# Optimization experiments

Hardware: AMD Instinct MI355X
Metric: run time of the kernel (lower is better)

Reference implementation:

```python
import jax, jax.numpy as jnp
import numpy as np
import math

N = 4096      # nodes
E = 131072    # edges
D = 256       # hidden / out_features
DIN = 16      # distance_map feature dim
H = 2         # attention heads
HD = D // H   # head dim = 128


def setup_inputs() -> dict:
    key = jax.random.key(0)
    ks = jax.random.split(key, 20)
    s = 0.02
    return {
        "input": jax.random.normal(ks[0], (N, D), jnp.float32),
        "adj": jax.random.randint(ks[1], (2, E), 0, N, jnp.int64),
        "h0": jax.random.normal(ks[2], (N, D), jnp.float32),
        "lamda": 1,
        "alpha": jax.random.uniform(ks[3], (1,), jnp.float32),
        "l": 1,
        "distance_map": jax.random.normal(ks[4], (E, DIN), jnp.float32),
        "norm": jax.random.uniform(ks[5], (E,), jnp.float32),
        # GraphConvolution params
        "weight_local": jax.random.normal(ks[6], (2 * D, D), jnp.float32) * s,
        "weight_global": jax.random.normal(ks[7], (2 * D, D), jnp.float32) * s,
        # EA_GCN.lin : Linear(16, D)
        "lin_w": jax.random.normal(ks[8], (D, DIN), jnp.float32) * s,
        "lin_b": jnp.zeros((D,), jnp.float32),
        # EA_GCN.W_EV : 3D -> 2D -> D -> 16 (GELU between)
        "w1": jax.random.normal(ks[9], (2 * D, 3 * D), jnp.float32) * s,
        "b1": jnp.zeros((2 * D,), jnp.float32),
        "w2": jax.random.normal(ks[10], (D, 2 * D), jnp.float32) * s,
        "b2": jnp.zeros((D,), jnp.float32),
        "w3": jax.random.normal(ks[11], (DIN, D), jnp.float32) * s,
        "b3": jnp.zeros((DIN,), jnp.float32),
        # MultiheadAttention params (torch layout: in_proj [3D, D])
        "in_proj_w": jax.random.normal(ks[12], (3 * D, D), jnp.float32) * s,
        "in_proj_b": jnp.zeros((3 * D,), jnp.float32),
        "out_proj_w": jax.random.normal(ks[13], (D, D), jnp.float32) * s,
        "out_proj_b": jnp.zeros((D,), jnp.float32),
    }


def _mha(x, wi, bi, wo, bo):
    # torch MHA, unbatched (N, D) input, eval mode (dropout off)
    qkv = x @ wi.T + bi                      # [N, 3D]
    q, k, v = jnp.split(qkv, 3, axis=-1)
    q = q.reshape(N, H, HD).transpose(1, 0, 2)  # [H, N, HD]
    k = k.reshape(N, H, HD).transpose(1, 0, 2)
    v = v.reshape(N, H, HD).transpose(1, 0, 2)
    scores = jnp.einsum("hnd,hmd->hnm", q, k) / math.sqrt(HD)
    attn = jax.nn.softmax(scores, axis=-1)
    o = jnp.einsum("hnm,hmd->hnd", attn, v)     # [H, N, HD]
    o = o.transpose(1, 0, 2).reshape(N, D)
    return o @ wo.T + bo


def _ea_gcn(x, edge_index, norm, distance_map, lin_w, lin_b, w1, b1, w2, b2, w3, b3):
    src, dst = edge_index[0], edge_index[1]
    edge_attr = distance_map @ lin_w.T + lin_b               # [E, D]
    msg = norm[:, None] * (x[src] + edge_attr)               # gather + combine
    agg = jax.ops.segment_sum(msg, dst, num_segments=N)      # scatter-add
    x_out = agg + x
    h = jnp.concatenate([x_out[src], edge_attr, x_out[dst]], axis=-1)  # [E, 3D]
    h = jax.nn.gelu(h @ w1.T + b1, approximate=False)
    h = jax.nn.gelu(h @ w2.T + b2, approximate=False)
    dm_out = h @ w3.T + b3                                   # [E, 16]
    return x_out, dm_out


def reference(input, adj, h0, lamda, alpha, l, distance_map, norm,
              weight_local, weight_global, lin_w, lin_b,
              w1, b1, w2, b2, w3, b3,
              in_proj_w, in_proj_b, out_proj_w, out_proj_b):
    theta = min(1.0, math.log(lamda / l + 1.0))
    a = alpha[0]
    h_local, dm_out = _ea_gcn(input, adj, norm, distance_map,
                              lin_w, lin_b, w1, b1, w2, b2, w3, b3)
    h_global = _mha(input, in_proj_w, in_proj_b, out_proj_w, out_proj_b)
    support_local = jnp.concatenate([h_local, h0], axis=1)   # [N, 2D]
    r_local = (1.0 - a) * h_local + a * h0
    support_global = jnp.concatenate([h_global, h0], axis=1)
    r_global = (1.0 - a) * h_global + a * h0
    output_local = theta * (support_local @ weight_local) + (1.0 - theta) * r_local
    output_global = theta * (support_global @ weight_global) + (1.0 - theta) * r_global
    output = output_local + output_global                    # residual=False
    return (output, dm_out)
```

## Files before the change

kernel.cpp:

```cpp
#include <hip/hip_runtime.h>
#include <hip/hip_bf16.h>
#include <math.h>

constexpr int N_   = 4096;
constexpr int E_   = 131072;
constexpr int D_   = 256;
constexpr int DIN_ = 16;
constexpr int D3_  = 768;
constexpr int HD_  = 128;

typedef __bf16 bf16_8 __attribute__((ext_vector_type(8)));
typedef float  f32x4  __attribute__((ext_vector_type(4)));
typedef float  f32x4v __attribute__((ext_vector_type(4)));
typedef unsigned int u32x4 __attribute__((ext_vector_type(4)));

__device__ __forceinline__ unsigned short f2b(float f) {
  unsigned int u = __float_as_uint(f);
  u = u + 0x7fffu + ((u >> 16) & 1u);
  return (unsigned short)(u >> 16);
}
__device__ __forceinline__ float b2f(unsigned short s) {
  return __uint_as_float(((unsigned int)s) << 16);
}
__device__ __forceinline__ unsigned int pack2(unsigned short lo, unsigned short hi) {
// ... 256 lines not shown
    const unsigned short* __restrict__ inb, const unsigned short* __restrict__ wqb,
    const float* __restrict__ ipb, float* __restrict__ qkv) {
  __shared__ unsigned short sA[128][72];
  __shared__ unsigned short sB[128][72];
  const int b   = blockIdx.x;
  const int j0  = (b % 6) * 128;
  const int m0  = (b / 6) * 128;
  const int tid = threadIdx.x;
  const int lane = tid & 63, wv = tid >> 6;
  const int r16  = lane & 15, quad = lane >> 4;
  const int sr   = tid >> 1, sh = (tid & 1) * 32;

  const unsigned short* ra = inb + (size_t)(m0 + sr) * D_;
  const unsigned short* rb = wqb + (size_t)(j0 + sr) * D_;

  const f32x4 zz = {0.f, 0.f, 0.f, 0.f};
  f32x4 acc[2][8];
#pragma unroll
  for (int m = 0; m < 2; ++m)
#pragma unroll
    for (int n = 0; n < 8; ++n) acc[m][n] = zz;

  for (int ki = 0; ki < 4; ++ki) {
    __syncthreads();
    {
      const uint4* s    = (const uint4*)(ra + ki * 64 + sh);
      const uint4* bsrc = (const uint4*)(rb + ki * 64 + sh);
      uint4* da = (uint4*)&sA[sr][sh];
      uint4* db = (uint4*)&sB[sr][sh];
#pragma unroll
      for (int i = 0; i < 4; ++i) { da[i] = s[i]; db[i] = bsrc[i]; }
    }
    __syncthreads();
#pragma unroll
    for (int kk = 0; kk < 2; ++kk) {
      bf16_8 a0 = frag16(&sA[wv * 32 + r16][kk * 32 + quad * 8]);
      bf16_8 a1 = frag16(&sA[wv * 32 + 16 + r16][kk * 32 + quad * 8]);
#pragma unroll
      for (int n = 0; n < 8; ++n) {
        bf16_8 bf = frag16(&sB[n * 16 + r16][kk * 32 + quad * 8]);
        acc[0][n] = __builtin_amdgcn_mfma_f32_16x16x32_bf16(a0, bf, acc[0][n], 0, 0, 0);
        acc[1][n] = __builtin_amdgcn_mfma_f32_16x16x32_bf16(a1, bf, acc[1][n], 0, 0, 0);
      }
    }
  }
#pragma unroll
  for (int m = 0; m < 2; ++m)
#pragma unroll
    for (int n = 0; n < 8; ++n) {
      int col = j0 + n * 16 + r16;
      float bb = ipb[col];
#pragma unroll
      for (int rg = 0; rg < 4; ++rg) {
        int row = m0 + wv * 32 + m * 16 + quad * 4 + rg;
        qkv[(size_t)row * D3_ + col] = acc[m][n][rg] + bb;
      }
    }
}

__global__ __launch_bounds__(256) void k_node_pac(
    const unsigned short* __restrict__ xbp, const unsigned short* __restrict__ wb1,
    unsigned short* __restrict__ Pac) {
  __shared__ unsigned short sA[128][72];
  __shared__ unsigned short sB[128][72];
  const int b    = blockIdx.x;
  const int j0   = (b & 7) * 128;
  const int m0   = (b >> 3) * 128;
  const int side = j0 >> 9;
  const int jr   = j0 - side * 512;
  const int tid  = threadIdx.x;
  const int lane = tid & 63, wv = tid >> 6;
  const int r16  = lane & 15, quad = lane >> 4;
  const int sr   = tid >> 1, sh = (tid & 1) * 32;

  const unsigned short* ra = xbp + (size_t)(m0 + sr) * D_;
  const unsigned short* rb = wb1 + (size_t)(jr + sr) * 768 + side * 512;

  const f32x4 zz = {0.f, 0.f, 0.f, 0.f};
  f32x4 acc[2][8];
#pragma unroll
  for (int m = 0; m < 2; ++m)
#pragma unroll
    for (int n = 0; n < 8; ++n) acc[m][n] = zz;

  for (int ki = 0; ki < 4; ++ki) {
    __syncthreads();
    {
      const uint4* s    = (const uint4*)(ra + ki * 64 + sh);
      const uint4* bsrc = (const uint4*)(rb + ki * 64 + sh);
      uint4* da = (uint4*)&sA[sr][sh];
      uint4* db = (uint4*)&sB[sr][sh];
#pragma unroll
      for (int i = 0; i < 4; ++i) { da[i] = s[i]; db[i] = bsrc[i]; }
    }
    __syncthreads();
#pragma unroll
    for (int kk = 0; kk < 2; ++kk) {
      bf16_8 a0 = frag16(&sA[wv * 32 + r16][kk * 32 + quad * 8]);
      bf16_8 a1 = frag16(&sA[wv * 32 + 16 + r16][kk * 32 + quad * 8]);
#pragma unroll
      for (int n = 0; n < 8; ++n) {
        bf16_8 bf = frag16(&sB[n * 16 + r16][kk * 32 + quad * 8]);
        acc[0][n] = __builtin_amdgcn_mfma_f32_16x16x32_bf16(a0, bf, acc[0][n], 0, 0, 0);
        acc[1][n] = __builtin_amdgcn_mfma_f32_16x16x32_bf16(a1, bf, acc[1][n], 0, 0, 0);
      }
    }
  }
#pragma unroll
  for (int m = 0; m < 2; ++m)
#pragma unroll
    for (int n = 0; n < 8; ++n) {
      int col = j0 + n * 16 + r16;
#pragma unroll
      for (int rg = 0; rg < 4; ++rg) {
        int row = m0 + wv * 32 + m * 16 + quad * 4 + rg;
        Pac[(size_t)row * 1024 + col] = f2b(acc[m][n][rg]);
      }
    }
}

__global__ __launch_bounds__(256) void k_outproj_mfma(
    const unsigned short* __restrict__ attob, const unsigned short* __restrict__ opwb,
    const float* __restrict__ opb, float* __restrict__ hgl,
    unsigned short* __restrict__ hgb) {
  __shared__ unsigned short sA[128][72];
  __shared__ unsigned short sB[128][72];
  const int b   = blockIdx.x;
  const int j0  = (b & 1) * 128;
  const int m0  = (b >> 1) * 128;
  const int tid = threadIdx.x;
  const int lane = tid & 63, wv = tid >> 6;
  const int r16  = lane & 15, quad = lane >> 4;
  const int sr   = tid >> 1, sh = (tid & 1) * 32;

  const unsigned short* ra = attob + (size_t)(m0 + sr) * D_;
  const unsigned short* rb = opwb + (size_t)(j0 + sr) * D_;

  const f32x4 zz = {0.f, 0.f, 0.f, 0.f};
  f32x4 acc[2][8];
#pragma unroll
  for (int m = 0; m < 2; ++m)
#pragma unroll
    for (int n = 0; n < 8; ++n) acc[m][n] = zz;

  for (int ki = 0; ki < 4; ++ki) {
    __syncthreads();
    {
      const uint4* s    = (const uint4*)(ra + ki * 64 + sh);
      const uint4* bsrc = (const uint4*)(rb + ki * 64 + sh);
      uint4* da = (uint4*)&sA[sr][sh];
      uint4* db = (uint4*)&sB[sr][sh];
#pragma unroll
      for (int i = 0; i < 4; ++i) { da[i] = s[i]; db[i] = bsrc[i]; }
    }
    __syncthreads();
#pragma unroll
    for (int kk = 0; kk < 2; ++kk) {
      bf16_8 a0 = frag16(&sA[wv * 32 + r16][kk * 32 + quad * 8]);
      bf16_8 a1 = frag16(&sA[wv * 32 + 16 + r16][kk * 32 + quad * 8]);
#pragma unroll
      for (int n = 0; n < 8; ++n) {
        bf16_8 bf = frag16(&sB[n * 16 + r16][kk * 32 + quad * 8]);
        acc[0][n] = __builtin_amdgcn_mfma_f32_16x16x32_bf16(a0, bf, acc[0][n], 0, 0, 0);
        acc[1][n] = __builtin_amdgcn_mfma_f32_16x16x32_bf16(a1, bf, acc[1][n], 0, 0, 0);
      }
    }
  }
#pragma unroll
  for (int m = 0; m < 2; ++m)
#pragma unroll
    for (int n = 0; n < 8; ++n) {
      int col = j0 + n * 16 + r16;
      float bb = opb[col];
#pragma unroll
      for (int rg = 0; rg < 4; ++rg) {
        int row = m0 + wv * 32 + m * 16 + quad * 4 + rg;
        float v = acc[m][n][rg] + bb;
        size_t idx = (size_t)row * D_ + col;
        hgl[idx] = v;
        hgb[idx] = f2b(v);
      }
    }
}

__global__ __launch_bounds__(256) void k_final_mfma(
    const unsigned short* __restrict__ xbp, const unsigned short* __restrict__ h0b,
    const unsigned short* __restrict__ hgb,
    const unsigned short* __restrict__ wlT, const unsigned short* __restrict__ wgT,
    const float* __restrict__ hl, const float* __restrict__ hg, const float* __restrict__ h0,
    const float* __restrict__ alpha_p, const void* lamda_p, const void* l_p,
    float* __restrict__ out) {
  __shared__ unsigned short sA[128][72];
  __shared__ unsigned short sB[128][72];
  const int b   = blockIdx.x;
  const int j0  = (b & 1) * 128;
  const int m0  = (b >> 1) * 128;
  const int tid = threadIdx.x;
  const int lane = tid & 63, wv = tid >> 6;
  const int r16  = lane & 15, quad = lane >> 4;
  const int sr   = tid >> 1, sh = (tid & 1) * 32;

  const f32x4 zz = {0.f, 0.f, 0.f, 0.f};
  f32x4 acc[2][8];
#pragma unroll
  for (int m = 0; m < 2; ++m)
#pragma unroll
    for (int n = 0; n < 8; ++n) acc[m][n] = zz;

  const size_t arow = (size_t)(m0 + sr) * D_;
  const size_t brow = (size_t)(j0 + sr) * 512;

  for (int ki = 0; ki < 16; ++ki) {
    __syncthreads();
    {
      const int gc = ki * 64 + sh;
      const unsigned short* ap =
          (gc < 256) ? xbp + arow + gc
        : (gc < 512) ? h0b + arow + (gc - 256)
        : (gc < 768) ? hgb + arow + (gc - 512)
                     : h0b + arow + (gc - 768);
      const unsigned short* bp = (gc < 512) ? wlT + brow + gc : wgT + brow + (gc - 512);
      const uint4* s    = (const uint4*)ap;
      const uint4* bsrc = (const uint4*)bp;
      uint4* da = (uint4*)&sA[sr][sh];
      uint4* db = (uint4*)&sB[sr][sh];
#pragma unroll
      for (int i = 0; i < 4; ++i) { da[i] = s[i]; db[i] = bsrc[i]; }
    }
    __syncthreads();
#pragma unroll
    for (int kk = 0; kk < 2; ++kk) {
      bf16_8 a0 = frag16(&sA[wv * 32 + r16][kk * 32 + quad * 8]);
      bf16_8 a1 = frag16(&sA[wv * 32 + 16 + r16][kk * 32 + quad * 8]);
#pragma unroll
      for (int n = 0; n < 8; ++n) {
        bf16_8 bf = frag16(&sB[n * 16 + r16][kk * 32 + quad * 8]);
        acc[0][n] = __builtin_amdgcn_mfma_f32_16x16x32_bf16(a0, bf, acc[0][n], 0, 0, 0);
        acc[1][n] = __builtin_amdgcn_mfma_f32_16x16x32_bf16(a1, bf, acc[1][n], 0, 0, 0);
      }
    }
  }
  float theta = fminf(1.f, logf(scalar_as_float(lamda_p) / scalar_as_float(l_p) + 1.f));
  float a = alpha_p[0];
  float omt = 1.f - theta;
#pragma unroll
  for (int m = 0; m < 2; ++m)
#pragma unroll
    for (int n = 0; n < 8; ++n) {
      int col = j0 + n * 16 + r16;
#pragma unroll
      for (int rg = 0; rg < 4; ++rg) {
        int row = m0 + wv * 32 + m * 16 + quad * 4 + rg;
        size_t idx = (size_t)row * D_ + col;
        out[idx] = theta * acc[m][n][rg] +
                   omt * ((1.f - a) * (hl[idx] + hg[idx]) + 2.f * a * h0[idx]);
      }
    }
}

__global__ void k_qk2b(const float* __restrict__ qkv,
                       unsigned short* __restrict__ Qb, unsigned short* __restrict__ Kb) {
  int off = (blockIdx.x * 256 + threadIdx.x) * 8;
  int n = off >> 9, c = off & 511;
  const float* src = qkv + (size_t)n * D3_ + c;
  float4 a = *(const float4*)src;
  float4 b = *(const float4*)(src + 4);
  uint4 p = {pack2(f2b(a.x), f2b(a.y)), pack2(f2b(a.z), f2b(a.w)),
             pack2(f2b(b.x), f2b(b.y)), pack2(f2b(b.z), f2b(b.w))};
  int cc = c & 255;
  int hh = cc >> 7, d = cc & 127;
  unsigned short* dst = (c < 256 ? Qb : Kb) + (size_t)hh * N_ * HD_ + (size_t)n * HD_ + d;
  *(uint4*)dst = p;
}

__global__ __launch_bounds__(256) void k_v2t(const float* __restrict__ qkv,
                                             unsigned short* __restrict__ Vt) {
  __shared__ unsigned short sv[64][136];
  int h = blockIdx.y;
  int n0 = blockIdx.x * 64;
  int tid = threadIdx.x;
#pragma unroll
  for (int it = 0; it < 4; ++it) {
    int off = (tid + it * 256) * 8;
    int r = off >> 7, d = off & 127;
    const float* src = qkv + (size_t)(n0 + r) * D3_ + 2 * D_ + h * HD_ + d;
    float4 a = *(const float4*)src;
    float4 b = *(const float4*)(src + 4);
    uint4 p = {pack2(f2b(a.x), f2b(a.y)), pack2(f2b(a.z), f2b(a.w)),
               pack2(f2b(b.x), f2b(b.y)), pack2(f2b(b.z), f2b(b.w))};
    *(uint4*)&sv[r][d] = p;
  }
  __syncthreads();
#pragma unroll
  for (int it = 0; it < 4; ++it) {
    int off = (tid + it * 256) * 8;
    int d = off >> 6, k = off & 63;
    unsigned short t[8];
#pragma unroll
    for (int j = 0; j < 8; ++j) t[j] = sv[k + j][d];
    uint4 p = {pack2(t[0], t[1]), pack2(t[2], t[3]),
               pack2(t[4], t[5]), pack2(t[6], t[7])};
    *(uint4*)(Vt + (size_t)h * HD_ * N_ + (size_t)d * N_ + n0 + k) = p;
  }
}

__global__ __launch_bounds__(256) void k_attn_mfma(
    const unsigned short* __restrict__ Qb, const unsigned short* __restrict__ Kb,
    const unsigned short* __restrict__ Vt, float* __restrict__ o_out,
    unsigned short* __restrict__ ob) {
  __shared__ unsigned short sK[64][136];
  __shared__ unsigned short sV[128][72];
  __shared__ float          sS[16][68];
  __shared__ unsigned short sP[16][72];
  __shared__ float sm[16], sl[16], sa[16];

  const int tid  = threadIdx.x;
  const int h    = blockIdx.y;
  const int q0   = blockIdx.x * 16;
  const int lane = tid & 63;
  const int wv   = tid >> 6;
  const int r16  = lane & 15;
  const int quad = lane >> 4;

  bf16_8 qf[4];
#pragma unroll
  for (int kk = 0; kk < 4; ++kk)
    qf[kk] = frag16(Qb + (size_t)h * N_ * HD_ + (size_t)(q0 + r16) * HD_ + kk * 32 + quad * 8);

  if (tid < 16) { sm[tid] = -1e30f; sl[tid] = 0.f; }

  const f32x4 zz = {0.f, 0.f, 0.f, 0.f};
  f32x4 o0 = zz, o1 = zz;

  const unsigned short* Kh = Kb + (size_t)h * N_ * HD_;
  const unsigned short* Vh = Vt + (size_t)h * HD_ * N_;

  for (int c0 = 0; c0 < N_; c0 += 64) {
    __syncthreads();
#pragma unroll
    for (int it = 0; it < 4; ++it) {
      int off = (tid + it * 256) * 8;
      int key = off >> 7, d = off & 127;
      *(uint4*)&sK[key][d] = *(const uint4*)(Kh + (size_t)(c0 + key) * HD_ + d);
    }
#pragma unroll
    for (int it = 0; it < 4; ++it) {
      int off = (tid + it * 256) * 8;
      int d = off >> 6, k = off & 63;
      *(uint4*)&sV[d][k] = *(const uint4*)(Vh + (size_t)d * N_ + c0 + k);
    }
    __syncthreads();
    f32x4 s = zz;
#pragma unroll
    for (int kk = 0; kk < 4; ++kk) {
      bf16_8 bf = frag16(&sK[wv * 16 + r16][kk * 32 + quad * 8]);
      s = __builtin_amdgcn_mfma_f32_16x16x32_bf16(qf[kk], bf, s, 0, 0, 0);
    }
    const float sc = 0.08838834764831845f;
#pragma unroll
    for (int r = 0; r < 4; ++r)
      sS[quad * 4 + r][wv * 16 + r16] = s[r] * sc;
    __syncthreads();
    {
      int row = tid >> 4, i = tid & 15;
      float4 v = *(const float4*)&sS[row][i * 4];
      float mx = fmaxf(fmaxf(v.x, v.y), fmaxf(v.z, v.w));
#pragma unroll
      for (int m = 1; m <= 8; m <<= 1) mx = fmaxf(mx, __shfl_xor(mx, m));
      float mo = sm[row];
      float mn = fmaxf(mo, mx);
      float p0 = __expf(v.x - mn), p1 = __expf(v.y - mn);
      float p2 = __expf(v.z - mn), p3 = __expf(v.w - mn);
      float ps = p0 + p1 + p2 + p3;
#pragma unroll
      for (int m = 1; m <= 8; m <<= 1) ps += __shfl_xor(ps, m);
      uint2 pk = {pack2(f2b(p0), f2b(p1)), pack2(f2b(p2), f2b(p3))};
      *(uint2*)&sP[row][i * 4] = pk;
      if (i == 0) {
        float al = __expf(mo - mn);
        sl[row] = sl[row] * al + ps;
        sm[row] = mn;
        sa[row] = al;
      }
    }
    __syncthreads();
    {
      float al0 = sa[quad * 4 + 0], al1 = sa[quad * 4 + 1];
      float al2 = sa[quad * 4 + 2], al3 = sa[quad * 4 + 3];
      o0[0] *= al0; o0[1] *= al1; o0[2] *= al2; o0[3] *= al3;
      o1[0] *= al0; o1[1] *= al1; o1[2] *= al2; o1[3] *= al3;
#pragma unroll
      for (int kk = 0; kk < 2; ++kk) {
        bf16_8 pa = frag16(&sP[r16][kk * 32 + quad * 8]);
        bf16_8 v0 = frag16(&sV[wv * 32 + r16][kk * 32 + quad * 8]);
        bf16_8 v1 = frag16(&sV[wv * 32 + 16 + r16][kk * 32 + quad * 8]);
        o0 = __builtin_amdgcn_mfma_f32_16x16x32_bf16(pa, v0, o0, 0, 0, 0);
        o1 = __builtin_amdgcn_mfma_f32_16x16x32_bf16(pa, v1, o1, 0, 0, 0);
      }
    }
  }
  {
    float i0 = 1.f / sl[quad * 4 + 0], i1 = 1.f / sl[quad * 4 + 1];
    float i2 = 1.f / sl[quad * 4 + 2], i3 = 1.f / sl[quad * 4 + 3];
    float vv[8];
    vv[0] = o0[0] * i0; vv[1] = o0[1] * i1; vv[2] = o0[2] * i2; vv[3] = o0[3] * i3;
    vv[4] = o1[0] * i0; vv[5] = o1[1] * i1; vv[6] = o1[2] * i2; vv[7] = o1[3] * i3;
#pragma unroll
    for (int g = 0; g < 2; ++g)
#pragma unroll
      for (int rg = 0; rg < 4; ++rg) {
        size_t idx = (size_t)(q0 + quad * 4 + rg) * D_ + h * HD_ + wv * 32 + g * 16 + r16;
        float v = vv[g * 4 + rg];
        o_out[idx] = v;
        ob[idx] = f2b(v);
      }
  }
}

__global__ __launch_bounds__(256) void k_final(
    const float* __restrict__ hl, const float* __restrict__ hg, const float* __restrict__ h0,
    const float* __restrict__ Wl, const float* __restrict__ Wg,
    const float* __restrict__ alpha_p, const void* lamda_p, const void* l_p,
    float* __restrict__ out) {
  __shared__ float sA[16][68];
  __shared__ float sB[16][68];
  float theta = fminf(1.f, logf(scalar_as_float(lamda_p) / scalar_as_float(l_p) + 1.f));
  float a = alpha_p[0];
  int bm = blockIdx.y * 64, bn = blockIdx.x * 64;
  int tid = threadIdx.x, tr = tid >> 4, tc = tid & 15;
  float acc[4][4] = {};
  for (int k0 = 0; k0 < 1024; k0 += 16) {
    for (int i = tid; i < 1024; i += 256) {
      int r = i >> 4, c = i & 15;
      int k = k0 + c;
      const float* src = (k < 256) ? hl : (k < 512) ? h0 : (k < 768) ? hg : h0;
      sA[c][r] = src[(size_t)(bm + r) * 256 + (k & 255)];
    }
    for (int i = tid; i < 1024; i += 256) {
      int kk = i >> 6, j = i & 63;
      int k = k0 + kk;
      const float* Bp = (k < 512) ? (Wl + (size_t)k * 256) : (Wg + (size_t)(k - 512) * 256);
      sB[kk][j] = Bp[bn + j];
    }
    __syncthreads();
#pragma unroll
    for (int kk = 0; kk < 16; kk++) {
      float av[4], bv[4];
#pragma unroll
      for (int i = 0; i < 4; i++) av[i] = sA[kk][tr * 4 + i];
#pragma unroll
      for (int j = 0; j < 4; j++) bv[j] = sB[kk][tc * 4 + j];
#pragma unroll
      for (int i = 0; i < 4; i++)
#pragma unroll
        for (int j = 0; j < 4; j++) acc[i][j] += av[i] * bv[j];
    }
    __syncthreads();
  }
  float omt = 1.f - theta;
#pragma unroll
  for (int i = 0; i < 4; i++) {
    int r = bm + tr * 4 + i;
#pragma unroll
    for (int j = 0; j < 4; j++) {
      int c = bn + tc * 4 + j;
      size_t idx = (size_t)r * 256 + c;
      out[idx] = theta * acc[i][j] + omt * ((1.f - a) * (hl[idx] + hg[idx]) + 2.f * a * h0[idx]);
    }
  }
}

__global__ __launch_bounds__(256, 4) void k_mlp_gemm1c(
    const float* __restrict__ dmap, const int* __restrict__ adj,
    const unsigned short* __restrict__ Pac, const unsigned short* __restrict__ Mb,
    const float* __restrict__ cbv, unsigned short* __restrict__ t1) {
  __shared__ unsigned short shm[8704];
  const int b    = blockIdx.x;
  const int c0   = (b >> 10) * 128;
  const int e0   = (b & 1023) * 128;
  const int tid  = threadIdx.x;
  const int lane = tid & 63, wv = tid >> 6;
  const int r16  = lane & 15, quad = lane >> 4;

  const uint4 z4 = make_uint4(0u, 0u, 0u, 0u);
  bf16_8 af[2];
#pragma unroll
  for (int m = 0; m < 2; ++m) {
    uint4 p = z4;
    if (quad < 2) {
      const int edge = e0 + wv * 32 + m * 16 + r16;
      const float4* dp = (const float4*)(dmap + (size_t)edge * DIN_ + quad * 8);
      float4 a = dp[0], bq = dp[1];
      p = make_uint4(pack2(f2b(a.x), f2b(a.y)), pack2(f2b(a.z), f2b(a.w)),
                     pack2(f2b(bq.x), f2b(bq.y)), pack2(f2b(bq.z), f2b(bq.w)));
    }
    af[m] = __builtin_bit_cast(bf16_8, p);
  }

  const f32x4 zz = {0.f, 0.f, 0.f, 0.f};
  f32x4 acc[2][8];
#pragma unroll
  for (int n = 0; n < 8; ++n) {
    uint4 mv = z4;
    if (quad < 2)
      mv = *(const uint4*)(Mb + (size_t)(c0 + n * 16 + r16) * DIN_ + quad * 8);
    bf16_8 bf = __builtin_bit_cast(bf16_8, mv);
    acc[0][n] = __builtin_amdgcn_mfma_f32_16x16x32_bf16(af[0], bf, zz, 0, 0, 0);
    acc[1][n] = __builtin_amdgcn_mfma_f32_16x16x32_bf16(af[1], bf, zz, 0, 0, 0);
  }

  unsigned short* reg = shm + wv * 2176;
#pragma unroll
  for (int m = 0; m < 2; ++m) {
#pragma unroll
    for (int n = 0; n < 8; ++n)
#pragma unroll
      for (int rg = 0; rg < 4; ++rg)
        reg[(quad * 4 + rg) * 136 + n * 16 + r16] = f2b(acc[m][n][rg]);
#pragma unroll
    for (int it = 0; it < 4; ++it) {
      int flat = it * 64 + lane;
      int row = flat >> 4;
      int g   = flat & 15;
      int er  = e0 + wv * 32 + m * 16 + row;
      int vs  = adj[er];
      int vd  = adj[E_ + er];
      int c   = c0 + g * 8;
      uint4 midq = *(const uint4*)&reg[row * 136 + g * 8];
      uint4 paq  = *(const uint4*)(Pac + (size_t)vs * 1024 + c);
      uint4 pcq  = *(const uint4*)(Pac + (size_t)vd * 1024 + 512 + c);
      float4 ba = *(const float4*)(cbv + c);
      float4 bb = *(const float4*)(cbv + c + 4);
      const unsigned int mv[4] = {midq.x, midq.y, midq.z, midq.w};
      const unsigned int pv[4] = {paq.x, paq.y, paq.z, paq.w};
      const unsigned int cv[4] = {pcq.x, pcq.y, pcq.z, pcq.w};
      const float bl[8] = {ba.x, ba.y, ba.z, ba.w, bb.x, bb.y, bb.z, bb.w};
      unsigned short us[8];
#pragma unroll
      for (int j = 0; j < 8; ++j) {
        unsigned short mw = (j & 1) ? (unsigned short)(mv[j >> 1] >> 16)
                                    : (unsigned short)(mv[j >> 1] & 0xffffu);
        unsigned short pw = (j & 1) ? (unsigned short)(pv[j >> 1] >> 16)
                                    : (unsigned short)(pv[j >> 1] & 0xffffu);
        unsigned short cw = (j & 1) ? (unsigned short)(cv[j >> 1] >> 16)
                                    : (unsigned short)(cv[j >> 1] & 0xffffu);
        float v = b2f(mw) + b2f(pw) + b2f(cw) + bl[j];
        us[j] = f2b(gelu_fast(v));
      }
      uint4 ov = make_uint4(pack2(us[0], us[1]), pack2(us[2], us[3]),
                            pack2(us[4], us[5]), pack2(us[6], us[7]));
      ntstore16(&t1[(size_t)er * 512 + c], ov);
    }
  }
}

__global__ __launch_bounds__(256, 2) void k_mlp_gemm23(
    const unsigned short* __restrict__ t1, const unsigned short* __restrict__ wb2,
    const float* __restrict__ b2, const unsigned short* __restrict__ wb3,
    const float* __restrict__ b3, float* __restrict__ dmo) {
  __shared__ unsigned short shm[24576];
  unsigned short* lA = shm;
  unsigned short* lB = shm + 8192;
  const int e0   = blockIdx.x * 128;
  const int tid  = threadIdx.x;
  const int lane = tid & 63, wv = tid >> 6;
  const int r16  = lane & 15, quad = lane >> 4;

  const int row0 = e0 + wv * 32 + r16;
  const int row1 = row0 + 16;
  const unsigned short* pa0 = t1 + (size_t)row0 * 512 + quad * 8;
  const unsigned short* pa1 = t1 + (size_t)row1 * 512 + quad * 8;

  const f32x4 zz = {0.f, 0.f, 0.f, 0.f};
  f32x4 acc[2][16];
#pragma unroll
  for (int m = 0; m < 2; ++m)
#pragma unroll
    for (int n = 0; n < 16; ++n) acc[m][n] = zz;

  for (int ki = 0; ki < 8; ++ki) {
    __syncthreads();
    {
#pragma unroll
      for (int kk = 0; kk < 2; ++kk) {
        gl2lds16(pa0 + ki * 64 + kk * 32, &lA[(wv * 4 + kk) * 512]);
        gl2lds16(pa1 + ki * 64 + kk * 32, &lA[(wv * 4 + 2 + kk) * 512]);
#pragma unroll
        for (int i = 0; i < 4; ++i) {
          int n = wv * 4 + i;
          gl2lds16(wb2 + (size_t)(n * 16 + r16) * 512 + ki * 64 + kk * 32 + quad * 8,
                   &lB[(n * 2 + kk) * 512]);
        }
      }
    }
    __builtin_amdgcn_s_waitcnt(0);
    __syncthreads();
#pragma unroll
    for (int kk = 0; kk < 2; ++kk) {
      bf16_8 a0 = frag16(&lA[(wv * 4 + kk) * 512 + lane * 8]);
      bf16_8 a1 = frag16(&lA[(wv * 4 + 2 + kk) * 512 + lane * 8]);
#pragma unroll
      for (int n = 0; n < 16; ++n) {
        bf16_8 bf = frag16(&lB[(n * 2 + kk) * 512 + lane * 8]);
        acc[0][n] = __builtin_amdgcn_mfma_f32_16x16x32_bf16(a0, bf, acc[0][n], 0, 0, 0);
        acc[1][n] = __builtin_amdgcn_mfma_f32_16x16x32_bf16(a1, bf, acc[1][n], 0, 0, 0);
      }
    }
  }
  __syncthreads();
  unsigned short* reg = shm + wv * 4224;
  float bb3 = b3[r16];
#pragma unroll
  for (int m = 0; m < 2; ++m) {
#pragma unroll
    for (int n = 0; n < 16; ++n) {
      float bb = b2[n * 16 + r16];
#pragma unroll
      for (int rg = 0; rg < 4; ++rg)
        reg[(quad * 4 + rg) * 264 + n * 16 + r16] = f2b(gelu_fast(acc[m][n][rg] + bb));
    }
    f32x4 acc3 = zz;
#pragma unroll
    for (int ks = 0; ks < 8; ++ks) {
      bf16_8 a = frag16(&reg[r16 * 264 + ks * 32 + quad * 8]);
      bf16_8 b = frag16(wb3 + (size_t)r16 * 256 + ks * 32 + quad * 8);
      acc3 = __builtin_amdgcn_mfma_f32_16x16x32_bf16(a, b, acc3, 0, 0, 0);
    }
#pragma unroll
    for (int rg = 0; rg < 4; ++rg)
      dmo[(size_t)(e0 + wv * 32 + m * 16 + quad * 4 + rg) * DIN_ + r16] = acc3[rg] + bb3;
  }
}

__global__ __launch_bounds__(256, 3) void k_edge_mlp_mfma(
    const float* __restrict__ xout, const int* __restrict__ adj,
    const float* __restrict__ dmap,
    const float* __restrict__ lin_w, const float* __restrict__ lin_b,
    const unsigned short* __restrict__ wb1, const float* __restrict__ b1,
    const unsigned short* __restrict__ wb2, const float* __restrict__ b2,
    const unsigned short* __restrict__ wb3, const float* __restrict__ b3,
    float* __restrict__ dmo) {
  __shared__ unsigned short sLo[8448];
  __shared__ unsigned short sT1[32][520];
  unsigned short (*sA)[136]  = (unsigned short(*)[136])sLo;
  unsigned short (*sT2)[264] = (unsigned short(*)[264])sLo;

  const int tid  = threadIdx.x;
  const int e0   = blockIdx.x * 32;
  const int lane = tid & 63;
  const int wv   = tid >> 6;
  const int r16  = lane & 15;
  const int quad = lane >> 4;

  const int sr = tid >> 3;
  const int t8 = tid & 7;
  const int se = e0 + sr;
  const int vsrc = adj[se];
  const int vdst = adj[E_ + se];

  float4 pf0, pf1, pf2, pf3;
  float4 dm0, dm1, dm2, dm3;
  {
    const float4* sp = (const float4*)(xout + (size_t)vsrc * D_ + t8 * 16);
    pf0 = sp[0]; pf1 = sp[1]; pf2 = sp[2]; pf3 = sp[3];
  }

  const f32x4 zz = {0.f, 0.f, 0.f, 0.f};
  f32x4 acc1[8][2];
#pragma unroll
  for (int i = 0; i < 8; ++i) { acc1[i][0] = zz; acc1[i][1] = zz; }

  for (int c = 0; c < 6; ++c) {
    const int k0 = c * 128;
    __syncthreads();
    {
      unsigned short tmp[16];
      if (c == 2 || c == 3) {
        int jb = (c - 2) * 128 + t8 * 16;
#pragma unroll
        for (int j = 0; j < 16; ++j) {
          const float4* lw = (const float4*)(lin_w + (size_t)(jb + j) * DIN_);
          float4 w0 = lw[0], w1 = lw[1], w2 = lw[2], w3 = lw[3];
          float acc = lin_b[jb + j];
          acc += dm0.x * w0.x + dm0.y * w0.y + dm0.z * w0.z + dm0.w * w0.w;
          acc += dm1.x * w1.x + dm1.y * w1.y + dm1.z * w1.z + dm1.w * w1.w;
          acc += dm2.x * w2.x + dm2.y * w2.y + dm2.z * w2.z + dm2.w * w2.w;
          acc += dm3.x * w3.x + dm3.y * w3.y + dm3.z * w3.z + dm3.w * w3.w;
          tmp[j] = f2b(acc);
        }
      } else {
        tmp[0]  = f2b(pf0.x); tmp[1]  = f2b(pf0.y); tmp[2]  = f2b(pf0.z); tmp[3]  = f2b(pf0.w);
        tmp[4]  = f2b(pf1.x); tmp[5]  = f2b(pf1.y); tmp[6]  = f2b(pf1.z); tmp[7]  = f2b(pf1.w);
        tmp[8]  = f2b(pf2.x); tmp[9]  = f2b(pf2.y); tmp[10] = f2b(pf2.z); tmp[11] = f2b(pf2.w);
        tmp[12] = f2b(pf3.x); tmp[13] = f2b(pf3.y); tmp[14] = f2b(pf3.z); tmp[15] = f2b(pf3.w);
      }
      unsigned short* dstp = &sA[sr][t8 * 16];
      uint4 q0v = {pack2(tmp[0], tmp[1]),   pack2(tmp[2], tmp[3]),
                   pack2(tmp[4], tmp[5]),   pack2(tmp[6], tmp[7])};
      uint4 q1v = {pack2(tmp[8], tmp[9]),   pack2(tmp[10], tmp[11]),
                   pack2(tmp[12], tmp[13]), pack2(tmp[14], tmp[15])};
      *(uint4*)(dstp) = q0v;
      *(uint4*)(dstp + 8) = q1v;
    }
    if (c == 0) {
      const float4* sp = (const float4*)(xout + (size_t)vsrc * D_ + 128 + t8 * 16);
      pf0 = sp[0]; pf1 = sp[1]; pf2 = sp[2]; pf3 = sp[3];
    } else if (c == 1) {
      const float4* dp = (const float4*)(dmap + (size_t)se * DIN_);
      dm0 = ntload4(dp); dm1 = ntload4(dp + 1); dm2 = ntload4(dp + 2); dm3 = ntload4(dp + 3);
    } else if (c == 3) {
      const float4* sp = (const float4*)(xout + (size_t)vdst * D_ + t8 * 16);
      pf0 = sp[0]; pf1 = sp[1]; pf2 = sp[2]; pf3 = sp[3];
    } else if (c == 4) {
      const float4* sp = (const float4*)(xout + (size_t)vdst * D_ + 128 + t8 * 16);
      pf0 = sp[0]; pf1 = sp[1]; pf2 = sp[2]; pf3 = sp[3];
    }
    __syncthreads();
#pragma unroll
    for (int kk = 0; kk < 4; ++kk) {
      bf16_8 a0 = frag16(&sA[r16][kk * 32 + quad * 8]);
      bf16_8 a1 = frag16(&sA[16 + r16][kk * 32 + quad * 8]);
#pragma unroll
      for (int i = 0; i < 8; ++i) {
        const unsigned short* bp =
            wb1 + (size_t)(wv * 128 + i * 16 + r16) * 768 + k0 + kk * 32 + quad * 8;
        bf16_8 bf = frag16(bp);
        acc1[i][0] = __builtin_amdgcn_mfma_f32_16x16x32_bf16(a0, bf, acc1[i][0], 0, 0, 0);
        acc1[i][1] = __builtin_amdgcn_mfma_f32_16x16x32_bf16(a1, bf, acc1[i][1], 0, 0, 0);
      }
    }
  }
#pragma unroll
  for (int i = 0; i < 8; ++i) {
    int col = wv * 128 + i * 16 + r16;
    float bb = b1[col];
#pragma unroll
    for (int r = 0; r < 4; ++r) {
      int row = quad * 4 + r;
      sT1[row][col] = f2b(gelu_exact(acc1[i][0][r] + bb));
      sT1[row + 16][col] = f2b(gelu_exact(acc1[i][1][r] + bb));
    }
  }
  __syncthreads();

  f32x4 acc2[4][2];
#pragma unroll
  for (int i = 0; i < 4; ++i) { acc2[i][0] = zz; acc2[i][1] = zz; }
#pragma unroll 4
  for (int ks = 0; ks < 16; ++ks) {
    bf16_8 a0 = frag16(&sT1[r16][ks * 32 + quad * 8]);
    bf16_8 a1 = frag16(&sT1[16 + r16][ks * 32 + quad * 8]);
#pragma unroll
    for (int i = 0; i < 4; ++i) {
      const unsigned short* bp =
          wb2 + (size_t)(wv * 64 + i * 16 + r16) * 512 + ks * 32 + quad * 8;
      bf16_8 bf = frag16(bp);
      acc2[i][0] = __builtin_amdgcn_mfma_f32_16x16x32_bf16(a0, bf, acc2[i][0], 0, 0, 0);
      acc2[i][1] = __builtin_amdgcn_mfma_f32_16x16x32_bf16(a1, bf, acc2[i][1], 0, 0, 0);
    }
  }
#pragma unroll
  for (int i = 0; i < 4; ++i) {
    int col = wv * 64 + i * 16 + r16;
    float bb = b2[col];
#pragma unroll
    for (int m = 0; m < 2; ++m)
#pragma unroll
      for (int r = 0; r < 4; ++r) {
        int row = m * 16 + quad * 4 + r;
        sT2[row][col] = f2b(gelu_exact(acc2[i][m][r] + bb));
      }
  }
  __syncthreads();

  if (wv < 2) {
    f32x4 acc3 = zz;
#pragma unroll
    for (int ks = 0; ks < 8; ++ks) {
      bf16_8 a = frag16(&sT2[wv * 16 + r16][ks * 32 + quad * 8]);
      bf16_8 b = frag16(wb3 + (size_t)r16 * 256 + ks * 32 + quad * 8);
      acc3 = __builtin_amdgcn_mfma_f32_16x16x32_bf16(a, b, acc3, 0, 0, 0);
    }
    float bb = b3[r16];
#pragma unroll
    for (int r = 0; r < 4; ++r) {
      int row = wv * 16 + quad * 4 + r;
      __builtin_nontemporal_store(acc3[r] + bb, &dmo[(size_t)(e0 + row) * DIN_ + r16]);
    }
  }
}

extern "C" void kernel_launch(void* const* d_in, const int* in_sizes, int n_in,
                              void* d_out, int out_size, void* d_ws, size_t ws_size,
                              hipStream_t stream) {
  const float* input = (const float*)d_in[0];
  const int*   adj   = (const int*)d_in[1];
  const float* h0    = (const float*)d_in[2];
  const void*  lamda = d_in[3];
  const float* alpha = (const float*)d_in[4];
  const void*  lll   = d_in[5];
  const float* dmap  = (const float*)d_in[6];
  const float* nrm   = (const float*)d_in[7];
  const float* Wl    = (const float*)d_in[8];
  const float* Wg    = (const float*)d_in[9];
  const float* lin_w = (const float*)d_in[10];
  const float* lin_b = (const float*)d_in[11];
  const float* w1    = (const float*)d_in[12];
  const float* b1    = (const float*)d_in[13];
  const float* w2    = (const float*)d_in[14];
  const float* b2    = (const float*)d_in[15];
  const float* w3    = (const float*)d_in[16];
  const float* b3    = (const float*)d_in[17];
  const float* ipw   = (const float*)d_in[18];
  const float* ipb   = (const float*)d_in[19];
  const float* opw   = (const float*)d_in[20];
  const float* opb   = (const float*)d_in[21];
  float* out = (float*)d_out;
  float* dmo = out + (size_t)N_ * D_;

  float* ws   = (float*)d_ws;
  float* xout = ws;
  float* qkv  = xout + (size_t)N_ * D_;
  float* atto = qkv  + (size_t)N_ * 3 * D_;
  float* hgl  = atto + (size_t)N_ * D_;
  unsigned short* wb1 = (unsigned short*)(hgl + (size_t)N_ * D_);
  unsigned short* wb2 = wb1 + 512 * 768;
  unsigned short* wb3 = wb2 + 256 * 512;
  unsigned short* Qb  = wb3 + 16 * 256;
  unsigned short* Kb  = Qb + 2 * N_ * HD_;
  unsigned short* Vt  = Kb + 2 * N_ * HD_;
  unsigned short* t1b = Vt + 2 * HD_ * N_;
  unsigned short* t2b = t1b + (size_t)E_ * 512;
  int* cnt  = (int*)(t2b + (size_t)E_ * 256);
  int* off  = cnt + 4096;
  int* cur  = off + 4100;
  int* perm = cur + 4096;
  unsigned short* xbp = (unsigned short*)(perm + E_);
  unsigned short* lwb = xbp + (size_t)N_ * D_;
  unsigned short* inb = lwb + 256 * DIN_;
  unsigned short* h0b = inb + (size_t)N_ * D_;
  unsigned short* hgb = h0b + (size_t)N_ * D_;
  unsigned short* wqb = hgb + (size_t)N_ * D_;
  unsigned short* wlT = wqb + 768 * 256;
  unsigned short* wgT = wlT + 256 * 512;
  unsigned short* opwb = wgT + 256 * 512;
  unsigned short* attob = (unsigned short*)qkv;
  unsigned short* Pac = (unsigned short*)qkv;
  unsigned short* Mb_ = t2b;
  float* cbv = (float*)(t2b + 8192);
  const size_t fast_need = (size_t)((char*)(opwb + 256 * 256) - (char*)d_ws);
  const bool fast = ws_size >= fast_need;

  if (fast) {
    k_prep_w<<<dim3((794624 + 255) / 256), 256, 0, stream>>>(
        w1, w2, w3, lin_w, ipw, opw, wb1, wb2, wb3, lwb, wqb, opwb);
    k_prep_t<<<dim3((262144 + 255) / 256), 256, 0, stream>>>(Wl, Wg, wlT, wgT);
    k_prep_x<<<dim3((2097152 + 255) / 256), 256, 0, stream>>>(input, h0, inb, h0b);
    k_prep_m<<<dim3(32), 256, 0, stream>>>(w1, lin_w, lin_b, b1, Mb_, cbv);

    k_zero<<<dim3(16), 256, 0, stream>>>(cnt, 4096);
    k_hist<<<dim3(E_ / 256), 256, 0, stream>>>(adj, cnt);
    k_scan<<<dim3(1), 1024, 0, stream>>>(cnt, off, cur);
    k_bucket<<<dim3(E_ / 256), 256, 0, stream>>>(adj, cur, perm);
    k_gather<<<dim3(N_), 256, 0, stream>>>(input, adj, dmap, nrm, lin_w, lin_b,
                                           off, perm, xout);
    k_f2b<<<dim3(N_ * D_ / 256), 256, 0, stream>>>(xout, xbp, N_ * D_);

    k_qkv_mfma<<<dim3(192), 256, 0, stream>>>(inb, wqb, ipb, qkv);
    k_qk2b<<<dim3(N_ * 512 / 8 / 256), 256, 0, stream>>>(qkv, Qb, Kb);
    k_v2t<<<dim3(N_ / 64, 2), 256, 0, stream>>>(qkv, Vt);
    k_attn_mfma<<<dim3(N_ / 16, 2), 256, 0, stream>>>(Qb, Kb, Vt, atto, attob);
    k_outproj_mfma<<<dim3(64), 256, 0, stream>>>(attob, opwb, opb, hgl, hgb);

    k_final_mfma<<<dim3(64), 256, 0, stream>>>(xbp, h0b, hgb, wlT, wgT,
                                               xout, hgl, h0, alpha, lamda, lll, out);

    k_node_pac<<<dim3(256), 256, 0, stream>>>(xbp, wb1, Pac);
    k_mlp_gemm1c<<<dim3(E_ / 128 * 4), 256, 0, stream>>>(dmap, adj, Pac, Mb_, cbv, t1b);
    k_mlp_gemm23<<<dim3(E_ / 128), 256, 0, stream>>>(t1b, wb2, b2, wb3, b3, dmo);
  } else {
    k_f2b<<<dim3((512 * 768 + 255) / 256), 256, 0, stream>>>(w1, wb1, 512 * 768);
    k_f2b<<<dim3((256 * 512 + 255) / 256), 256, 0, stream>>>(w2, wb2, 256 * 512);
    k_f2b<<<dim3((16 * 256 + 255) / 256), 256, 0, stream>>>(w3, wb3, 16 * 256);
    k_copy4<<<dim3(N_ * D_ / 4 / 256), 256, 0, stream>>>((const float4*)input, (float4*)xout,
                                                         N_ * D_ / 4);
    k_scatter<<<dim3(E_ / 4), 256, 0, stream>>>(input, adj, dmap, nrm, lin_w, lin_b, xout);
    k_gemm_bt<<<dim3(D3_ / 64, N_ / 64), 256, 0, stream>>>(input, ipw, ipb, qkv, N_, D3_, D_);
    k_qk2b<<<dim3(N_ * 512 / 8 / 256), 256, 0, stream>>>(qkv, Qb, Kb);
    k_v2t<<<dim3(N_ / 64, 2), 256, 0, stream>>>(qkv, Vt);
    k_attn_mfma<<<dim3(N_ / 16, 2), 256, 0, stream>>>(Qb, Kb, Vt, atto, (unsigned short*)qkv);
    k_gemm_bt<<<dim3(D_ / 64, N_ / 64), 256, 0, stream>>>(atto, opw, opb, hgl, N_, D_, D_);
    k_final<<<dim3(4, N_ / 64), 256, 0, stream>>>(xout, hgl, h0, Wl, Wg, alpha, lamda, lll, out);
    k_edge_mlp_mfma<<<dim3(E_ / 32), 256, 0, stream>>>(xout, adj, dmap, lin_w, lin_b,
                                                       wb1, b1, wb2, b2, wb3, b3, dmo);
  }
}
```

Before: 528.8 us.

## Split attention over key halves and merge partial softmax results

Replaces the single-pass flash attention kernel with a split-K variant: each block handles 16 queries over half of the keys, writing unnormalized partial outputs plus running max and sum. A separate combine kernel rescales and merges the two halves, producing both the fp32 and bf16 attention outputs. This doubles the grid from 512 to 1024 blocks to improve occupancy across CUs. In exchange it adds an extra launch and extra global traffic for the fp32 partials.

```diff
diff --git a/kernel.cpp b/kernel.cpp
--- a/kernel.cpp
+++ b/kernel.cpp
@@ -582,6 +582,138 @@
                pack2(t[4], t[5]), pack2(t[6], t[7])};
     *(uint4*)(Vt + (size_t)h * HD_ * N_ + (size_t)d * N_ + n0 + k) = p;
   }
+}
+
+__global__ __launch_bounds__(256) void k_attn_split(
+    const unsigned short* __restrict__ Qb, const unsigned short* __restrict__ Kb,
+    const unsigned short* __restrict__ Vt, float* __restrict__ po,
+    float* __restrict__ pml) {
+  __shared__ unsigned short sK[64][136];
+  __shared__ unsigned short sV[128][72];
+  __shared__ float          sS[16][68];
+  __shared__ unsigned short sP[16][72];
+  __shared__ float sm[16], sl[16], sa[16];
+
+  const int tid  = threadIdx.x;
+  const int h    = blockIdx.y >> 1;
+  const int kr   = blockIdx.y & 1;
+  const int q0   = blockIdx.x * 16;
+  const int lane = tid & 63;
+  const int wv   = tid >> 6;
+  const int r16  = lane & 15;
+  const int quad = lane >> 4;
+
+  bf16_8 qf[4];
+#pragma unroll
+  for (int kk = 0; kk < 4; ++kk)
+    qf[kk] = frag16(Qb + (size_t)h * N_ * HD_ + (size_t)(q0 + r16) * HD_ + kk * 32 + quad * 8);
+
+  if (tid < 16) { sm[tid] = -1e30f; sl[tid] = 0.f; }
+
+  const f32x4 zz = {0.f, 0.f, 0.f, 0.f};
+  f32x4 o0 = zz, o1 = zz;
+
+  const unsigned short* Kh = Kb + (size_t)h * N_ * HD_;
+  const unsigned short* Vh = Vt + (size_t)h * HD_ * N_;
+
+  const int cbeg = kr * (N_ / 2);
+  for (int c0 = cbeg; c0 < cbeg + N_ / 2; c0 += 64) {
+    __syncthreads();
+#pragma unroll
+    for (int it = 0; it < 4; ++it) {
+      int off = (tid + it * 256) * 8;
+      int key = off >> 7, d = off & 127;
+      *(uint4*)&sK[key][d] = *(const uint4*)(Kh + (size_t)(c0 + key) * HD_ + d);
+    }
+#pragma unroll
+    for (int it = 0; it < 4; ++it) {
+      int off = (tid + it * 256) * 8;
+      int d = off >> 6, k = off & 63;
+      *(uint4*)&sV[d][k] = *(const uint4*)(Vh + (size_t)d * N_ + c0 + k);
+    }
+    __syncthreads();
+    f32x4 s = zz;
+#pragma unroll
+    for (int kk = 0; kk < 4; ++kk) {
+      bf16_8 bf = frag16(&sK[wv * 16 + r16][kk * 32 + quad * 8]);
+      s = __builtin_amdgcn_mfma_f32_16x16x32_bf16(qf[kk], bf, s, 0, 0, 0);
+    }
+    const float sc = 0.08838834764831845f;
+#pragma unroll
+    for (int r = 0; r < 4; ++r)
+      sS[quad * 4 + r][wv * 16 + r16] = s[r] * sc;
+    __syncthreads();
+    {
+      int row = tid >> 4, i = tid & 15;
+      float4 v = *(const float4*)&sS[row][i * 4];
+      float mx = fmaxf(fmaxf(v.x, v.y), fmaxf(v.z, v.w));
+#pragma unroll
+      for (int m = 1; m <= 8; m <<= 1) mx = fmaxf(mx, __shfl_xor(mx, m));
+      float mo = sm[row];
+      float mn = fmaxf(mo, mx);
+      float p0 = __expf(v.x - mn), p1 = __expf(v.y - mn);
+      float p2 = __expf(v.z - mn), p3 = __expf(v.w - mn);
+      float ps = p0 + p1 + p2 + p3;
+#pragma unroll
+      for (int m = 1; m <= 8; m <<= 1) ps += __shfl_xor(ps, m);
+      uint2 pk = {pack2(f2b(p0), f2b(p1)), pack2(f2b(p2), f2b(p3))};
+      *(uint2*)&sP[row][i * 4] = pk;
+      if (i == 0) {
+        float al = __expf(mo - mn);
+        sl[row] = sl[row] * al + ps;
+        sm[row] = mn;
+        sa[row] = al;
+      }
+    }
+    __syncthreads();
+    {
+      float al0 = sa[quad * 4 + 0], al1 = sa[quad * 4 + 1];
+      float al2 = sa[quad * 4 + 2], al3 = sa[quad * 4 + 3];
+      o0[0] *= al0; o0[1] *= al1; o0[2] *= al2; o0[3] *= al3;
+      o1[0] *= al0; o1[1] *= al1; o1[2] *= al2; o1[3] *= al3;
+#pragma unroll
+      for (int kk = 0; kk < 2; ++kk) {
+        bf16_8 pa = frag16(&sP[r16][kk * 32 + quad * 8]);
+        bf16_8 v0 = frag16(&sV[wv * 32 + r16][kk * 32 + quad * 8]);
+        bf16_8 v1 = frag16(&sV[wv * 32 + 16 + r16][kk * 32 + quad * 8]);
+        o0 = __builtin_amdgcn_mfma_f32_16x16x32_bf16(pa, v0, o0, 0, 0, 0);
+        o1 = __builtin_amdgcn_mfma_f32_16x16x32_bf16(pa, v1, o1, 0, 0, 0);
+      }
+    }
+  }
+  {
+    const size_t base = ((size_t)(kr * 2 + h) * N_ + q0);
+#pragma unroll
+    for (int g = 0; g < 2; ++g)
+#pragma unroll
+      for (int rg = 0; rg < 4; ++rg) {
+        size_t idx = (base + quad * 4 + rg) * HD_ + wv * 32 + g * 16 + r16;
+        po[idx] = (g ? o1 : o0)[rg];
+      }
+    if (tid < 16) {
+      pml[(base + tid) * 2 + 0] = sm[tid];
+      pml[(base + tid) * 2 + 1] = sl[tid];
+    }
+  }
+}
+
+__global__ void k_attn_comb(const float* __restrict__ po, const float* __restrict__ pml,
+                            float* __restrict__ atto, unsigned short* __restrict__ attob) {
+  int i = blockIdx.x * 256 + threadIdx.x;
+  int d = i & 127;
+  int n = (i >> 7) & (N_ - 1);
+  int h = i >> 19;
+  size_t r0 = (size_t)(0 * 2 + h) * N_ + n;
+  size_t r1 = (size_t)(1 * 2 + h) * N_ + n;
+  float m0 = pml[r0 * 2 + 0], l0 = pml[r0 * 2 + 1];
+  float m1 = pml[r1 * 2 + 0], l1 = pml[r1 * 2 + 1];
+  float m = fmaxf(m0, m1);
+  float e0 = __expf(m0 - m), e1 = __expf(m1 - m);
+  float denom = l0 * e0 + l1 * e1;
+  float o = (po[r0 * HD_ + d] * e0 + po[r1 * HD_ + d] * e1) / denom;
+  size_t idx = (size_t)n * D_ + h * HD_ + d;
+  atto[idx] = o;
+  attob[idx] = f2b(o);
 }
 
 __global__ __launch_bounds__(256) void k_attn_mfma(
@@ -1128,6 +1260,8 @@
   unsigned short* Pac = (unsigned short*)qkv;
   unsigned short* Mb_ = t2b;
   float* cbv = (float*)(t2b + 8192);
+  float* po  = (float*)(t2b + 32768);
+  float* pml = po + (size_t)4 * N_ * HD_;
   const size_t fast_need = (size_t)((char*)(opwb + 256 * 256) - (char*)d_ws);
   const bool fast = ws_size >= fast_need;
 
@@ -1149,7 +1283,8 @@
     k_qkv_mfma<<<dim3(192), 256, 0, stream>>>(inb, wqb, ipb, qkv);
     k_qk2b<<<dim3(N_ * 512 / 8 / 256), 256, 0, stream>>>(qkv, Qb, Kb);
     k_v2t<<<dim3(N_ / 64, 2), 256, 0, stream>>>(qkv, Vt);
-    k_attn_mfma<<<dim3(N_ / 16, 2), 256, 0, stream>>>(Qb, Kb, Vt, atto, attob);
+    k_attn_split<<<dim3(N_ / 16, 4), 256, 0, stream>>>(Qb, Kb, Vt, po, pml);
+    k_attn_comb<<<dim3(2 * N_ * HD_ / 256), 256, 0, stream>>>(po, pml, atto, attob);
     k_outproj_mfma<<<dim3(64), 256, 0, stream>>>(attob, opwb, opb, hgl, hgb);
 
     k_final_mfma<<<dim3(64), 256, 0, stream>>>(xbp, h0b, hgb, wlT, wgT,
```

After: 533.8 us. Within noise of the previous version (+0.9%).

## Fuse edge MLP first layer into second GEMM, dropping t1 intermediate

Applied to the files above, without the earlier changes.

Merges the first edge-MLP layer (distance-map MFMA plus gathered node projections, bias and GELU) into the second-layer GEMM kernel. The A tile is now produced in registers and written straight to LDS each k-step instead of being loaded from a bf16 t1 buffer in global memory. This removes a write and re-read of a 131072x512 bf16 intermediate and one kernel launch. In exchange the GEMM loop carries more ALU and gather work per step, and uses more LDS per block.

```diff
diff --git a/kernel.cpp b/kernel.cpp
--- a/kernel.cpp
+++ b/kernel.cpp
@@ -750,95 +750,14 @@
   }
 }
 
-__global__ __launch_bounds__(256, 4) void k_mlp_gemm1c(
+__global__ __launch_bounds__(256, 2) void k_mlp_f23(
     const float* __restrict__ dmap, const int* __restrict__ adj,
     const unsigned short* __restrict__ Pac, const unsigned short* __restrict__ Mb,
-    const float* __restrict__ cbv, unsigned short* __restrict__ t1) {
-  __shared__ unsigned short shm[8704];
-  const int b    = blockIdx.x;
-  const int c0   = (b >> 10) * 128;
-  const int e0   = (b & 1023) * 128;
-  const int tid  = threadIdx.x;
-  const int lane = tid & 63, wv = tid >> 6;
-  const int r16  = lane & 15, quad = lane >> 4;
-
-  const uint4 z4 = make_uint4(0u, 0u, 0u, 0u);
-  bf16_8 af[2];
-#pragma unroll
-  for (int m = 0; m < 2; ++m) {
-    uint4 p = z4;
-    if (quad < 2) {
-      const int edge = e0 + wv * 32 + m * 16 + r16;
-      const float4* dp = (const float4*)(dmap + (size_t)edge * DIN_ + quad * 8);
-      float4 a = dp[0], bq = dp[1];
-      p = make_uint4(pack2(f2b(a.x), f2b(a.y)), pack2(f2b(a.z), f2b(a.w)),
-                     pack2(f2b(bq.x), f2b(bq.y)), pack2(f2b(bq.z), f2b(bq.w)));
-    }
-    af[m] = __builtin_bit_cast(bf16_8, p);
-  }
-
-  const f32x4 zz = {0.f, 0.f, 0.f, 0.f};
-  f32x4 acc[2][8];
-#pragma unroll
-  for (int n = 0; n < 8; ++n) {
-    uint4 mv = z4;
-    if (quad < 2)
-      mv = *(const uint4*)(Mb + (size_t)(c0 + n * 16 + r16) * DIN_ + quad * 8);
-    bf16_8 bf = __builtin_bit_cast(bf16_8, mv);
-    acc[0][n] = __builtin_amdgcn_mfma_f32_16x16x32_bf16(af[0], bf, zz, 0, 0, 0);
-    acc[1][n] = __builtin_amdgcn_mfma_f32_16x16x32_bf16(af[1], bf, zz, 0, 0, 0);
-  }
-
-  unsigned short* reg = shm + wv * 2176;
-#pragma unroll
-  for (int m = 0; m < 2; ++m) {
-#pragma unroll
-    for (int n = 0; n < 8; ++n)
-#pragma unroll
-      for (int rg = 0; rg < 4; ++rg)
-        reg[(quad * 4 + rg) * 136 + n * 16 + r16] = f2b(acc[m][n][rg]);
-#pragma unroll
-    for (int it = 0; it < 4; ++it) {
-      int flat = it * 64 + lane;
-      int row = flat >> 4;
-      int g   = flat & 15;
-      int er  = e0 + wv * 32 + m * 16 + row;
-      int vs  = adj[er];
-      int vd  = adj[E_ + er];
-      int c   = c0 + g * 8;
-      uint4 midq = *(const uint4*)&reg[row * 136 + g * 8];
-      uint4 paq  = *(const uint4*)(Pac + (size_t)vs * 1024 + c);
-      uint4 pcq  = *(const uint4*)(Pac + (size_t)vd * 1024 + 512 + c);
-      float4 ba = *(const float4*)(cbv + c);
-      float4 bb = *(const float4*)(cbv + c + 4);
-      const unsigned int mv[4] = {midq.x, midq.y, midq.z, midq.w};
-      const unsigned int pv[4] = {paq.x, paq.y, paq.z, paq.w};
-      const unsigned int cv[4] = {pcq.x, pcq.y, pcq.z, pcq.w};
-      const float bl[8] = {ba.x, ba.y, ba.z, ba.w, bb.x, bb.y, bb.z, bb.w};
-      unsigned short us[8];
-#pragma unroll
-      for (int j = 0; j < 8; ++j) {
-        unsigned short mw = (j & 1) ? (unsigned short)(mv[j >> 1] >> 16)
-                                    : (unsigned short)(mv[j >> 1] & 0xffffu);
-        unsigned short pw = (j & 1) ? (unsigned short)(pv[j >> 1] >> 16)
-                                    : (unsigned short)(pv[j >> 1] & 0xffffu);
-        unsigned short cw = (j & 1) ? (unsigned short)(cv[j >> 1] >> 16)
-                                    : (unsigned short)(cv[j >> 1] & 0xffffu);
-        float v = b2f(mw) + b2f(pw) + b2f(cw) + bl[j];
-        us[j] = f2b(gelu_fast(v));
-      }
-      uint4 ov = make_uint4(pack2(us[0], us[1]), pack2(us[2], us[3]),
-                            pack2(us[4], us[5]), pack2(us[6], us[7]));
-      ntstore16(&t1[(size_t)er * 512 + c], ov);
-    }
-  }
-}
-
-__global__ __launch_bounds__(256, 2) void k_mlp_gemm23(
-    const unsigned short* __restrict__ t1, const unsigned short* __restrict__ wb2,
-    const float* __restrict__ b2, const unsigned short* __restrict__ wb3,
-    const float* __restrict__ b3, float* __restrict__ dmo) {
-  __shared__ unsigned short shm[24576];
+    const float* __restrict__ cbv,
+    const unsigned short* __restrict__ wb2, const float* __restrict__ b2,
+    const unsigned short* __restrict__ wb3, const float* __restrict__ b3,
+    float* __restrict__ dmo) {
+  __shared__ unsigned short shm[29440];
   unsigned short* lA = shm;
   unsigned short* lB = shm + 8192;
   const int e0   = blockIdx.x * 128;
@@ -846,10 +765,31 @@
   const int lane = tid & 63, wv = tid >> 6;
   const int r16  = lane & 15, quad = lane >> 4;
 
-  const int row0 = e0 + wv * 32 + r16;
-  const int row1 = row0 + 16;
-  const unsigned short* pa0 = t1 + (size_t)row0 * 512 + quad * 8;
-  const unsigned short* pa1 = t1 + (size_t)row1 * 512 + quad * 8;
+  const int er0 = e0 + wv * 32 + r16;
+  const int er1 = er0 + 16;
+  const int vs0 = adj[er0], vs1 = adj[er1];
+  const int vd0 = adj[E_ + er0], vd1 = adj[E_ + er1];
+  const unsigned short* pA0 = Pac + (size_t)vs0 * 1024;
+  const unsigned short* pA1 = Pac + (size_t)vs1 * 1024;
+  const unsigned short* pC0 = Pac + (size_t)vd0 * 1024 + 512;
+  const unsigned short* pC1 = Pac + (size_t)vd1 * 1024 + 512;
+
+  const uint4 z4 = make_uint4(0u, 0u, 0u, 0u);
+  bf16_8 af[2];
+#pragma unroll
+  for (int m = 0; m < 2; ++m) {
+    uint4 p = z4;
+    if (quad < 2) {
+      const int edge = m ? er1 : er0;
+      const float4* dp = (const float4*)(dmap + (size_t)edge * DIN_ + quad * 8);
+      float4 a = dp[0], bq = dp[1];
+      p = make_uint4(pack2(f2b(a.x), f2b(a.y)), pack2(f2b(a.z), f2b(a.w)),
+                     pack2(f2b(bq.x), f2b(bq.y)), pack2(f2b(bq.z), f2b(bq.w)));
+    }
+    af[m] = __builtin_bit_cast(bf16_8, p);
+  }
+
+  unsigned short* sc = shm + 24576 + wv * 1216;
 
   const f32x4 zz = {0.f, 0.f, 0.f, 0.f};
   f32x4 acc[2][16];
@@ -860,17 +800,60 @@
 
   for (int ki = 0; ki < 8; ++ki) {
     __syncthreads();
-    {
-#pragma unroll
-      for (int kk = 0; kk < 2; ++kk) {
-        gl2lds16(pa0 + ki * 64 + kk * 32, &lA[(wv * 4 + kk) * 512]);
-        gl2lds16(pa1 + ki * 64 + kk * 32, &lA[(wv * 4 + 2 + kk) * 512]);
-#pragma unroll
-        for (int i = 0; i < 4; ++i) {
-          int n = wv * 4 + i;
-          gl2lds16(wb2 + (size_t)(n * 16 + r16) * 512 + ki * 64 + kk * 32 + quad * 8,
-                   &lB[(n * 2 + kk) * 512]);
+#pragma unroll
+    for (int kk = 0; kk < 2; ++kk)
+#pragma unroll
+      for (int i = 0; i < 4; ++i) {
+        int n = wv * 4 + i;
+        gl2lds16(wb2 + (size_t)(n * 16 + r16) * 512 + ki * 64 + kk * 32 + quad * 8,
+                 &lB[(n * 2 + kk) * 512]);
+      }
+    f32x4 am[2][4];
+#pragma unroll
+    for (int n = 0; n < 4; ++n) {
+      uint4 mv = z4;
+      if (quad < 2)
+        mv = *(const uint4*)(Mb + (size_t)(ki * 64 + n * 16 + r16) * DIN_ + quad * 8);
+      bf16_8 bf = __builtin_bit_cast(bf16_8, mv);
+      am[0][n] = __builtin_amdgcn_mfma_f32_16x16x32_bf16(af[0], bf, zz, 0, 0, 0);
+      am[1][n] = __builtin_amdgcn_mfma_f32_16x16x32_bf16(af[1], bf, zz, 0, 0, 0);
+    }
+#pragma unroll
+    for (int m = 0; m < 2; ++m) {
+#pragma unroll
+      for (int n = 0; n < 4; ++n)
+#pragma unroll
+        for (int rg = 0; rg < 4; ++rg)
+          sc[(quad * 4 + rg) * 76 + n * 16 + r16] = f2b(am[m][n][rg]);
+      const unsigned short* pa = m ? pA1 : pA0;
+      const unsigned short* pc = m ? pC1 : pC0;
+#pragma unroll
+      for (int it = 0; it < 2; ++it) {
+        const int c = ki * 64 + it * 32 + quad * 8;
+        uint4 midq = *(const uint4*)&sc[r16 * 76 + it * 32 + quad * 8];
+        uint4 paq  = *(const uint4*)(pa + c);
+        uint4 pcq  = *(const uint4*)(pc + c);
+        float4 ba = *(const float4*)(cbv + c);
+        float4 bb = *(const float4*)(cbv + c + 4);
+        const unsigned int mv[4] = {midq.x, midq.y, midq.z, midq.w};
+        const unsigned int pv[4] = {paq.x, paq.y, paq.z, paq.w};
+        const unsigned int cv[4] = {pcq.x, pcq.y, pcq.z, pcq.w};
+        const float bl[8] = {ba.x, ba.y, ba.z, ba.w, bb.x, bb.y, bb.z, bb.w};
+        unsigned short us[8];
+#pragma unroll
+        for (int j = 0; j < 8; ++j) {
+          unsigned short mw = (j & 1) ? (unsigned short)(mv[j >> 1] >> 16)
+                                      : (unsigned short)(mv[j >> 1] & 0xffffu);
+          unsigned short pw = (j & 1) ? (unsigned short)(pv[j >> 1] >> 16)
+                                      : (unsigned short)(pv[j >> 1] & 0xffffu);
+          unsigned short cw = (j & 1) ? (unsigned short)(cv[j >> 1] >> 16)
+                                      : (unsigned short)(cv[j >> 1] & 0xffffu);
+          float v = b2f(mw) + b2f(pw) + b2f(cw) + bl[j];
+          us[j] = f2b(gelu_fast(v));
         }
+        *(uint4*)&lA[(wv * 4 + m * 2 + it) * 512 + lane * 8] = make_uint4(
+            pack2(us[0], us[1]), pack2(us[2], us[3]),
+            pack2(us[4], us[5]), pack2(us[6], us[7]));
       }
     }
     __builtin_amdgcn_s_waitcnt(0);
@@ -1156,8 +1139,8 @@
                                                xout, hgl, h0, alpha, lamda, lll, out);
 
     k_node_pac<<<dim3(256), 256, 0, stream>>>(xbp, wb1, Pac);
-    k_mlp_gemm1c<<<dim3(E_ / 128 * 4), 256, 0, stream>>>(dmap, adj, Pac, Mb_, cbv, t1b);
-    k_mlp_gemm23<<<dim3(E_ / 128), 256, 0, stream>>>(t1b, wb2, b2, wb3, b3, dmo);
+    k_mlp_f23<<<dim3(E_ / 128), 256, 0, stream>>>(dmap, adj, Pac, Mb_, cbv,
+                                                  wb2, b2, wb3, b3, dmo);
   } else {
     k_f2b<<<dim3((512 * 768 + 255) / 256), 256, 0, stream>>>(w1, wb1, 512 * 768);
     k_f2b<<<dim3((256 * 512 + 255) / 256), 256, 0, stream>>>(w2, wb2, 256 * 512);
```

New measurement: 535.3 us. About the same (+1.2%).
